# Kernel tuning notes

Hardware: AMD Instinct MI355X
Metric: run time of the kernel (lower is better)

The kernel has to match this reference:

```python
import jax, jax.numpy as jnp
import numpy as np

NUM_USR = 8192
H = 256  # NUM_SOURCE == H (feature dim of y_a); NUM_TARGET = 256


def setup_inputs() -> dict:
    key = jax.random.key(0)
    k1, k2, k3, k4 = jax.random.split(key, 4)
    return {
        "y_a": jax.random.normal(k1, (NUM_USR, H), dtype=jnp.float32),
        "y_b": jax.random.normal(k2, (NUM_USR, H), dtype=jnp.float32),
        "W": jax.random.normal(k3, (H, H), dtype=jnp.float32) * (1.0 / np.sqrt(H)),
        "b": jax.random.normal(k4, (H,), dtype=jnp.float32) * 0.01,
    }


def reference(y_a, y_b, W, b):
    # Linear: proj[j] = W @ y_b[j] + b   (torch nn.Linear convention)
    proj = jnp.einsum("jt,st->js", y_b, W) + b          # [num_usr, H]
    # torch loop computes score[i, j] = y_a[i] . proj[j], replicated H times
    # then averaged: out[i, k] = (1/H) * sum_j sigmoid(score[i, j])
    scores = jnp.einsum("ih,jh->ij", y_a, proj)          # [num_usr, num_usr]
    s = jnp.sum(jax.nn.sigmoid(scores), axis=1) / y_a.shape[1]  # [num_usr]
    return jnp.broadcast_to(s[:, None], y_a.shape)       # [num_usr, H]
```

## Files before the change

### kernel.cpp

```cpp
#include <hip/hip_runtime.h>

#define NUSR 8192
#define HDIM 256

typedef __attribute__((ext_vector_type(8))) __bf16 bf16x8;
typedef __attribute__((ext_vector_type(4))) float f32x4;

union frag_u { bf16x8 v; unsigned short u[8]; };

__device__ __forceinline__ unsigned short f2bf(float f) {
  unsigned u = __builtin_bit_cast(unsigned, f);
  u += 0x7FFFu + ((u >> 16) & 1u);
  return (unsigned short)(u >> 16);
}

__device__ __forceinline__ float sigmoidf_fast(float x) {
  float e = __builtin_amdgcn_exp2f(x * -1.44269504088896340736f);
  return __builtin_amdgcn_rcpf(1.0f + e);
}

__global__ __launch_bounds__(256) void k1_proj(
    const float* __restrict__ yb, const float* __restrict__ W,
    const float* __restrict__ bvec, unsigned short* __restrict__ Pbf)
{
  const int tid  = threadIdx.x;
  const int lane = tid & 63;
  const int w    = tid >> 6;
  const int quad = lane >> 4;
  const int l15  = lane & 15;
  const int rb   = blockIdx.x * 32;

  frag_u A[2][8];
#pragma unroll
  for (int h = 0; h < 2; ++h) {
    const float* src = yb + (size_t)(rb + h * 16 + l15) * HDIM;
#pragma unroll
    for (int kb = 0; kb < 8; ++kb) {
      float4 v0 = *(const float4*)&src[kb * 32 + quad * 8];
      float4 v1 = *(const float4*)&src[kb * 32 + quad * 8 + 4];
      A[h][kb].u[0] = f2bf(v0.x); A[h][kb].u[1] = f2bf(v0.y);
      A[h][kb].u[2] = f2bf(v0.z); A[h][kb].u[3] = f2bf(v0.w);
      A[h][kb].u[4] = f2bf(v1.x); A[h][kb].u[5] = f2bf(v1.y);
      A[h][kb].u[6] = f2bf(v1.z); A[h][kb].u[7] = f2bf(v1.w);
    }
  }

#pragma unroll
  for (int tt = 0; tt < 4; ++tt) {
    const int scol = w * 64 + tt * 16 + l15;
    const float* wrow = W + (size_t)scol * HDIM;
    f32x4 a0 = {0.f,0.f,0.f,0.f}, a1 = {0.f,0.f,0.f,0.f};
#pragma unroll
    for (int kb = 0; kb < 8; ++kb) {
      float4 v0 = *(const float4*)&wrow[kb * 32 + quad * 8];
      float4 v1 = *(const float4*)&wrow[kb * 32 + quad * 8 + 4];
      frag_u B;
      B.u[0] = f2bf(v0.x); B.u[1] = f2bf(v0.y);
      B.u[2] = f2bf(v0.z); B.u[3] = f2bf(v0.w);
      B.u[4] = f2bf(v1.x); B.u[5] = f2bf(v1.y);
      B.u[6] = f2bf(v1.z); B.u[7] = f2bf(v1.w);
      a0 = __builtin_amdgcn_mfma_f32_16x16x32_bf16(A[0][kb].v, B.v, a0, 0, 0, 0);
      a1 = __builtin_amdgcn_mfma_f32_16x16x32_bf16(A[1][kb].v, B.v, a1, 0, 0, 0);
    }
    const float bcol = bvec[scol];
#pragma unroll
    for (int r = 0; r < 4; ++r) {
      Pbf[(size_t)(rb + quad * 4 + r) * HDIM + scol]      = f2bf(a0[r] + bcol);
      Pbf[(size_t)(rb + 16 + quad * 4 + r) * HDIM + scol] = f2bf(a1[r] + bcol);
    }
  }
}

__global__ __launch_bounds__(256) void k2_score(
    const float* __restrict__ ya, const unsigned short* __restrict__ Pbf,
    float* __restrict__ svec)
{
  __shared__ __align__(16) unsigned short bs[64 * 264];
  const int tid  = threadIdx.x;
  const int lane = tid & 63;
  const int w    = tid >> 6;
  const int quad = lane >> 4;
  const int l15  = lane & 15;
  const int rbase = blockIdx.x * 128 + w * 32;
  const int cbase = blockIdx.y * 512;

  frag_u A[2][8];
#pragma unroll
  for (int h = 0; h < 2; ++h) {
    const float* src = ya + (size_t)(rbase + h * 16 + l15) * HDIM;
#pragma unroll
    for (int kb = 0; kb < 8; ++kb) {
      float4 v0 = *(const float4*)&src[kb * 32 + quad * 8];
      float4 v1 = *(const float4*)&src[kb * 32 + quad * 8 + 4];
      A[h][kb].u[0] = f2bf(v0.x); A[h][kb].u[1] = f2bf(v0.y);
      A[h][kb].u[2] = f2bf(v0.z); A[h][kb].u[3] = f2bf(v0.w);
      A[h][kb].u[4] = f2bf(v1.x); A[h][kb].u[5] = f2bf(v1.y);
      A[h][kb].u[6] = f2bf(v1.z); A[h][kb].u[7] = f2bf(v1.w);
    }
  }

  float rs[2][4] = {{0.f,0.f,0.f,0.f},{0.f,0.f,0.f,0.f}};

  for (int st = 0; st < 8; ++st) {
    __syncthreads();
    {
      const uint4* src = (const uint4*)(Pbf + (size_t)(cbase + st * 64) * HDIM);
#pragma unroll
      for (int p = 0; p < 8; ++p) {
        int lin = p * 256 + tid;
        int row = lin >> 5, ch = lin & 31;
        *(uint4*)&bs[row * 264 + ch * 8] = src[row * 32 + ch];
      }
    }
    __syncthreads();
#pragma unroll
    for (int tt = 0; tt < 4; ++tt) {
      f32x4 a0 = {0.f,0.f,0.f,0.f}, a1 = {0.f,0.f,0.f,0.f};
#pragma unroll
      for (int kb = 0; kb < 8; ++kb) {
        bf16x8 bfrag = *(const bf16x8*)&bs[(tt * 16 + l15) * 264 + kb * 32 + quad * 8];
        a0 = __builtin_amdgcn_mfma_f32_16x16x32_bf16(A[0][kb].v, bfrag, a0, 0, 0, 0);
        a1 = __builtin_amdgcn_mfma_f32_16x16x32_bf16(A[1][kb].v, bfrag, a1, 0, 0, 0);
      }
#pragma unroll
      for (int r = 0; r < 4; ++r) {
        rs[0][r] += sigmoidf_fast(a0[r]);
        rs[1][r] += sigmoidf_fast(a1[r]);
      }
    }
  }

#pragma unroll
  for (int off = 1; off < 16; off <<= 1) {
#pragma unroll
    for (int h = 0; h < 2; ++h)
#pragma unroll
      for (int r = 0; r < 4; ++r)
        rs[h][r] += __shfl_xor(rs[h][r], off, 64);
  }
  if (l15 == 0) {
#pragma unroll
    for (int h = 0; h < 2; ++h)
#pragma unroll
      for (int r = 0; r < 4; ++r)
        atomicAdd(&svec[rbase + h * 16 + quad * 4 + r], rs[h][r]);
  }
}

__global__ __launch_bounds__(256) void k3_bcast(
    const float* __restrict__ svec, float* __restrict__ out)
{
  int idx = blockIdx.x * 256 + threadIdx.x;
  int row = idx >> 6;
  float v = svec[row] * (1.0f / 256.0f);
  float4 o = {v, v, v, v};
  ((float4*)out)[idx] = o;
}

extern "C" void kernel_launch(void* const* d_in, const int* in_sizes, int n_in,
                              void* d_out, int out_size, void* d_ws, size_t ws_size,
                              hipStream_t stream) {
  (void)in_sizes; (void)n_in; (void)out_size;
  const float* ya = (const float*)d_in[0];
  const float* yb = (const float*)d_in[1];
  const float* W  = (const float*)d_in[2];
  const float* bv = (const float*)d_in[3];
  float* out = (float*)d_out;

  char* ws = (char*)d_ws;
  unsigned short* Pbf;
  float* svec;
  const size_t need = (4ull << 20) + (32ull << 10);
  if (ws_size >= need) {
    Pbf  = (unsigned short*)ws;
    svec = (float*)(ws + (4 << 20));
  } else {
    Pbf  = (unsigned short*)d_out;
    svec = (float*)ws;
  }

  hipMemsetAsync(svec, 0, NUSR * sizeof(float), stream);
  k1_proj<<<256, 256, 0, stream>>>(yb, W, bv, Pbf);
  k2_score<<<dim3(64, 16), 256, 0, stream>>>(ya, Pbf, svec);
  k3_bcast<<<2048, 256, 0, stream>>>(svec, out);
}
```

Before: 131.8 us.

## Enlarge score row tile, split projection grid, fold memset into projection kernel

The score kernel now has each wave cover 64 rows instead of 32, so every B fragment read from shared memory feeds four MFMAs instead of two. The grid is halved and each block stages the same number of columns, which cuts global and LDS traffic per useful FLOP. The projection kernel moves to a 2D grid with one output tile per wave, which raises parallelism. It also zeroes svec, removing the separate memset launch, and the bf16 packing now converts two values per 32-bit word. In exchange the score kernel uses more registers and launches only 512 blocks, so occupancy and load balance may drop.

```diff
diff --git a/kernel.cpp b/kernel.cpp
--- a/kernel.cpp
+++ b/kernel.cpp
@@ -6,12 +6,16 @@
 typedef __attribute__((ext_vector_type(8))) __bf16 bf16x8;
 typedef __attribute__((ext_vector_type(4))) float f32x4;
 
-union frag_u { bf16x8 v; unsigned short u[8]; };
+union frag_u { bf16x8 v; unsigned short u[8]; unsigned int d[4]; };
 
-__device__ __forceinline__ unsigned short f2bf(float f) {
+__device__ __forceinline__ unsigned int f2bf(float f) {
   unsigned u = __builtin_bit_cast(unsigned, f);
   u += 0x7FFFu + ((u >> 16) & 1u);
-  return (unsigned short)(u >> 16);
+  return u >> 16;
+}
+
+__device__ __forceinline__ unsigned int f2bf2(float lo, float hi) {
+  return f2bf(lo) | (f2bf(hi) << 16);
 }
 
 __device__ __forceinline__ float sigmoidf_fast(float x) {
@@ -21,7 +25,8 @@
 
 __global__ __launch_bounds__(256) void k1_proj(
     const float* __restrict__ yb, const float* __restrict__ W,
-    const float* __restrict__ bvec, unsigned short* __restrict__ Pbf)
+    const float* __restrict__ bvec, unsigned short* __restrict__ Pbf,
+    float* __restrict__ svec)
 {
   const int tid  = threadIdx.x;
   const int lane = tid & 63;
@@ -29,6 +34,9 @@
   const int quad = lane >> 4;
   const int l15  = lane & 15;
   const int rb   = blockIdx.x * 32;
+  const int sb   = blockIdx.y * 64 + w * 16;
+
+  if (blockIdx.y == 0 && tid < 32) svec[rb + tid] = 0.f;
 
   frag_u A[2][8];
 #pragma unroll
@@ -38,40 +46,36 @@
     for (int kb = 0; kb < 8; ++kb) {
       float4 v0 = *(const float4*)&src[kb * 32 + quad * 8];
       float4 v1 = *(const float4*)&src[kb * 32 + quad * 8 + 4];
-      A[h][kb].u[0] = f2bf(v0.x); A[h][kb].u[1] = f2bf(v0.y);
-      A[h][kb].u[2] = f2bf(v0.z); A[h][kb].u[3] = f2bf(v0.w);
-      A[h][kb].u[4] = f2bf(v1.x); A[h][kb].u[5] = f2bf(v1.y);
-      A[h][kb].u[6] = f2bf(v1.z); A[h][kb].u[7] = f2bf(v1.w);
+      A[h][kb].d[0] = f2bf2(v0.x, v0.y);
+      A[h][kb].d[1] = f2bf2(v0.z, v0.w);
+      A[h][kb].d[2] = f2bf2(v1.x, v1.y);
+      A[h][kb].d[3] = f2bf2(v1.z, v1.w);
     }
   }
 
+  const float* wrow = W + (size_t)(sb + l15) * HDIM;
+  f32x4 a0 = {0.f,0.f,0.f,0.f}, a1 = {0.f,0.f,0.f,0.f};
 #pragma unroll
-  for (int tt = 0; tt < 4; ++tt) {
-    const int scol = w * 64 + tt * 16 + l15;
-    const float* wrow = W + (size_t)scol * HDIM;
-    f32x4 a0 = {0.f,0.f,0.f,0.f}, a1 = {0.f,0.f,0.f,0.f};
+  for (int kb = 0; kb < 8; ++kb) {
+    float4 v0 = *(const float4*)&wrow[kb * 32 + quad * 8];
+    float4 v1 = *(const float4*)&wrow[kb * 32 + quad * 8 + 4];
+    frag_u B;
+    B.d[0] = f2bf2(v0.x, v0.y);
+    B.d[1] = f2bf2(v0.z, v0.w);
+    B.d[2] = f2bf2(v1.x, v1.y);
+    B.d[3] = f2bf2(v1.z, v1.w);
+    a0 = __builtin_amdgcn_mfma_f32_16x16x32_bf16(A[0][kb].v, B.v, a0, 0, 0, 0);
+    a1 = __builtin_amdgcn_mfma_f32_16x16x32_bf16(A[1][kb].v, B.v, a1, 0, 0, 0);
+  }
+  const float bias = bvec[sb + l15];
 #pragma unroll
-    for (int kb = 0; kb < 8; ++kb) {
-      float4 v0 = *(const float4*)&wrow[kb * 32 + quad * 8];
-      float4 v1 = *(const float4*)&wrow[kb * 32 + quad * 8 + 4];
-      frag_u B;
-      B.u[0] = f2bf(v0.x); B.u[1] = f2bf(v0.y);
-      B.u[2] = f2bf(v0.z); B.u[3] = f2bf(v0.w);
-      B.u[4] = f2bf(v1.x); B.u[5] = f2bf(v1.y);
-      B.u[6] = f2bf(v1.z); B.u[7] = f2bf(v1.w);
-      a0 = __builtin_amdgcn_mfma_f32_16x16x32_bf16(A[0][kb].v, B.v, a0, 0, 0, 0);
-      a1 = __builtin_amdgcn_mfma_f32_16x16x32_bf16(A[1][kb].v, B.v, a1, 0, 0, 0);
-    }
-    const float bcol = bvec[scol];
-#pragma unroll
-    for (int r = 0; r < 4; ++r) {
-      Pbf[(size_t)(rb + quad * 4 + r) * HDIM + scol]      = f2bf(a0[r] + bcol);
-      Pbf[(size_t)(rb + 16 + quad * 4 + r) * HDIM + scol] = f2bf(a1[r] + bcol);
-    }
+  for (int r = 0; r < 4; ++r) {
+    Pbf[(size_t)(rb + quad * 4 + r) * HDIM + sb + l15]      = (unsigned short)f2bf(a0[r] + bias);
+    Pbf[(size_t)(rb + 16 + quad * 4 + r) * HDIM + sb + l15] = (unsigned short)f2bf(a1[r] + bias);
   }
 }
 
-__global__ __launch_bounds__(256) void k2_score(
+__global__ __launch_bounds__(256, 2) void k2_score(
     const float* __restrict__ ya, const unsigned short* __restrict__ Pbf,
     float* __restrict__ svec)
 {
@@ -81,25 +85,26 @@
   const int w    = tid >> 6;
   const int quad = lane >> 4;
   const int l15  = lane & 15;
-  const int rbase = blockIdx.x * 128 + w * 32;
+  const int rbase = blockIdx.x * 256 + w * 64;
   const int cbase = blockIdx.y * 512;
 
-  frag_u A[2][8];
+  frag_u A[4][8];
 #pragma unroll
-  for (int h = 0; h < 2; ++h) {
-    const float* src = ya + (size_t)(rbase + h * 16 + l15) * HDIM;
+  for (int g = 0; g < 4; ++g) {
+    const float* src = ya + (size_t)(rbase + g * 16 + l15) * HDIM;
 #pragma unroll
     for (int kb = 0; kb < 8; ++kb) {
       float4 v0 = *(const float4*)&src[kb * 32 + quad * 8];
       float4 v1 = *(const float4*)&src[kb * 32 + quad * 8 + 4];
-      A[h][kb].u[0] = f2bf(v0.x); A[h][kb].u[1] = f2bf(v0.y);
-      A[h][kb].u[2] = f2bf(v0.z); A[h][kb].u[3] = f2bf(v0.w);
-      A[h][kb].u[4] = f2bf(v1.x); A[h][kb].u[5] = f2bf(v1.y);
-      A[h][kb].u[6] = f2bf(v1.z); A[h][kb].u[7] = f2bf(v1.w);
+      A[g][kb].d[0] = f2bf2(v0.x, v0.y);
+      A[g][kb].d[1] = f2bf2(v0.z, v0.w);
+      A[g][kb].d[2] = f2bf2(v1.x, v1.y);
+      A[g][kb].d[3] = f2bf2(v1.z, v1.w);
     }
   }
 
-  float rs[2][4] = {{0.f,0.f,0.f,0.f},{0.f,0.f,0.f,0.f}};
+  float rs[4][4] = {{0.f,0.f,0.f,0.f},{0.f,0.f,0.f,0.f},
+                    {0.f,0.f,0.f,0.f},{0.f,0.f,0.f,0.f}};
 
   for (int st = 0; st < 8; ++st) {
     __syncthreads();
@@ -115,35 +120,37 @@
     __syncthreads();
 #pragma unroll
     for (int tt = 0; tt < 4; ++tt) {
-      f32x4 a0 = {0.f,0.f,0.f,0.f}, a1 = {0.f,0.f,0.f,0.f};
+      f32x4 acc[4] = {{0.f,0.f,0.f,0.f},{0.f,0.f,0.f,0.f},
+                      {0.f,0.f,0.f,0.f},{0.f,0.f,0.f,0.f}};
 #pragma unroll
       for (int kb = 0; kb < 8; ++kb) {
         bf16x8 bfrag = *(const bf16x8*)&bs[(tt * 16 + l15) * 264 + kb * 32 + quad * 8];
-        a0 = __builtin_amdgcn_mfma_f32_16x16x32_bf16(A[0][kb].v, bfrag, a0, 0, 0, 0);
-        a1 = __builtin_amdgcn_mfma_f32_16x16x32_bf16(A[1][kb].v, bfrag, a1, 0, 0, 0);
+#pragma unroll
+        for (int g = 0; g < 4; ++g)
+          acc[g] = __builtin_amdgcn_mfma_f32_16x16x32_bf16(A[g][kb].v, bfrag, acc[g], 0, 0, 0);
       }
 #pragma unroll
-      for (int r = 0; r < 4; ++r) {
-        rs[0][r] += sigmoidf_fast(a0[r]);
-        rs[1][r] += sigmoidf_fast(a1[r]);
-      }
+      for (int g = 0; g < 4; ++g)
+#pragma unroll
+        for (int r = 0; r < 4; ++r)
+          rs[g][r] += sigmoidf_fast(acc[g][r]);
     }
   }
 
 #pragma unroll
-  for (int off = 1; off < 16; off <<= 1) {
+  for (int off = 1; off < 16; off <<= 1)
 #pragma unroll
-    for (int h = 0; h < 2; ++h)
+    for (int g = 0; g < 4; ++g)
 #pragma unroll
       for (int r = 0; r < 4; ++r)
-        rs[h][r] += __shfl_xor(rs[h][r], off, 64);
-  }
+        rs[g][r] += __shfl_xor(rs[g][r], off, 64);
+
   if (l15 == 0) {
 #pragma unroll
-    for (int h = 0; h < 2; ++h)
+    for (int g = 0; g < 4; ++g)
 #pragma unroll
       for (int r = 0; r < 4; ++r)
-        atomicAdd(&svec[rbase + h * 16 + quad * 4 + r], rs[h][r]);
+        atomicAdd(&svec[rbase + g * 16 + quad * 4 + r], rs[g][r]);
   }
 }
 
@@ -179,8 +186,7 @@
     svec = (float*)ws;
   }
 
-  hipMemsetAsync(svec, 0, NUSR * sizeof(float), stream);
-  k1_proj<<<256, 256, 0, stream>>>(yb, W, bv, Pbf);
-  k2_score<<<dim3(64, 16), 256, 0, stream>>>(ya, Pbf, svec);
+  k1_proj<<<dim3(256, 4), 256, 0, stream>>>(yb, W, bv, Pbf, svec);
+  k2_score<<<dim3(32, 16), 256, 0, stream>>>(ya, Pbf, svec);
   k3_bcast<<<2048, 256, 0, stream>>>(svec, out);
 }
```

Result: slower. 144.9 us (+9.9%).

## Pre-swizzle projection into MFMA fragment layout, pre-convert y_a, async LDS loads

Applied to the files above, without the earlier changes.

The projection kernel now writes P in a fragment-ordered layout so the score kernel can copy tiles into LDS with global_load_lds and read B fragments contiguously per lane. The same kernel converts y_a to bf16 once and zeroes svec, which removes the separate memset and the repeated f32-to-bf16 conversion across the 16 column blocks of the score kernel. The projection kernel is restructured into 512 single-wave blocks that compute W·y_b with y_b as the resident operand. The costs are an extra 4 MB workspace buffer and a dependence on the exact fragment layout matching between the two kernels.

```diff
diff --git a/kernel.cpp b/kernel.cpp
--- a/kernel.cpp
+++ b/kernel.cpp
@@ -6,111 +6,115 @@
 typedef __attribute__((ext_vector_type(8))) __bf16 bf16x8;
 typedef __attribute__((ext_vector_type(4))) float f32x4;
 
-union frag_u { bf16x8 v; unsigned short u[8]; };
+union frag_u { bf16x8 v; unsigned short u[8]; unsigned int d[4]; };
 
-__device__ __forceinline__ unsigned short f2bf(float f) {
+__device__ __forceinline__ unsigned int f2bf(float f) {
   unsigned u = __builtin_bit_cast(unsigned, f);
   u += 0x7FFFu + ((u >> 16) & 1u);
-  return (unsigned short)(u >> 16);
+  return u >> 16;
 }
-
+__device__ __forceinline__ unsigned int f2bf2(float lo, float hi) {
+  return f2bf(lo) | (f2bf(hi) << 16);
+}
 __device__ __forceinline__ float sigmoidf_fast(float x) {
   float e = __builtin_amdgcn_exp2f(x * -1.44269504088896340736f);
   return __builtin_amdgcn_rcpf(1.0f + e);
 }
 
-__global__ __launch_bounds__(256) void k1_proj(
-    const float* __restrict__ yb, const float* __restrict__ W,
-    const float* __restrict__ bvec, unsigned short* __restrict__ Pbf)
+
+__global__ __launch_bounds__(64) void k1_proj(
+    const float* __restrict__ ya, const float* __restrict__ yb,
+    const float* __restrict__ W, const float* __restrict__ bvec,
+    unsigned short* __restrict__ PX, unsigned short* __restrict__ yabf,
+    float* __restrict__ svec)
 {
-  const int tid  = threadIdx.x;
-  const int lane = tid & 63;
-  const int w    = tid >> 6;
-  const int quad = lane >> 4;
-  const int l15  = lane & 15;
-  const int rb   = blockIdx.x * 32;
+  const int lane = threadIdx.x;
+  const int q = lane >> 4, i = lane & 15;
+  const int jg = blockIdx.x;
 
-  frag_u A[2][8];
+  {
+    const float4* src = (const float4*)ya;
+    uint4* dst = (uint4*)yabf;
 #pragma unroll
-  for (int h = 0; h < 2; ++h) {
-    const float* src = yb + (size_t)(rb + h * 16 + l15) * HDIM;
+    for (int u = 0; u < 8; ++u) {
+      int d = u * 32768 + jg * 64 + lane;
+      float4 a = src[d * 2];
+      float4 b = src[d * 2 + 1];
+      uint4 o = { f2bf2(a.x, a.y), f2bf2(a.z, a.w),
+                  f2bf2(b.x, b.y), f2bf2(b.z, b.w) };
+      dst[d] = o;
+    }
+  }
+  if (jg < 128) svec[jg * 64 + lane] = 0.f;
+
+  frag_u B[8];
+  {
+    const float* ybrow = yb + (size_t)(jg * 16 + i) * HDIM;
 #pragma unroll
     for (int kb = 0; kb < 8; ++kb) {
-      float4 v0 = *(const float4*)&src[kb * 32 + quad * 8];
-      float4 v1 = *(const float4*)&src[kb * 32 + quad * 8 + 4];
-      A[h][kb].u[0] = f2bf(v0.x); A[h][kb].u[1] = f2bf(v0.y);
-      A[h][kb].u[2] = f2bf(v0.z); A[h][kb].u[3] = f2bf(v0.w);
-      A[h][kb].u[4] = f2bf(v1.x); A[h][kb].u[5] = f2bf(v1.y);
-      A[h][kb].u[6] = f2bf(v1.z); A[h][kb].u[7] = f2bf(v1.w);
+      float4 v0 = *(const float4*)&ybrow[kb * 32 + q * 8];
+      float4 v1 = *(const float4*)&ybrow[kb * 32 + q * 8 + 4];
+      B[kb].d[0] = f2bf2(v0.x, v0.y); B[kb].d[1] = f2bf2(v0.z, v0.w);
+      B[kb].d[2] = f2bf2(v1.x, v1.y); B[kb].d[3] = f2bf2(v1.z, v1.w);
     }
   }
 
-#pragma unroll
-  for (int tt = 0; tt < 4; ++tt) {
-    const int scol = w * 64 + tt * 16 + l15;
-    const float* wrow = W + (size_t)scol * HDIM;
-    f32x4 a0 = {0.f,0.f,0.f,0.f}, a1 = {0.f,0.f,0.f,0.f};
+#pragma unroll 2
+  for (int st = 0; st < 16; ++st) {
+    f32x4 acc = {0.f, 0.f, 0.f, 0.f};
 #pragma unroll
     for (int kb = 0; kb < 8; ++kb) {
-      float4 v0 = *(const float4*)&wrow[kb * 32 + quad * 8];
-      float4 v1 = *(const float4*)&wrow[kb * 32 + quad * 8 + 4];
-      frag_u B;
-      B.u[0] = f2bf(v0.x); B.u[1] = f2bf(v0.y);
-      B.u[2] = f2bf(v0.z); B.u[3] = f2bf(v0.w);
-      B.u[4] = f2bf(v1.x); B.u[5] = f2bf(v1.y);
-      B.u[6] = f2bf(v1.z); B.u[7] = f2bf(v1.w);
-      a0 = __builtin_amdgcn_mfma_f32_16x16x32_bf16(A[0][kb].v, B.v, a0, 0, 0, 0);
-      a1 = __builtin_amdgcn_mfma_f32_16x16x32_bf16(A[1][kb].v, B.v, a1, 0, 0, 0);
+      const float* wrow = W + (size_t)(st * 16 + i) * HDIM + kb * 32 + q * 8;
+      float4 w0 = *(const float4*)wrow;
+      float4 w1 = *(const float4*)(wrow + 4);
+      frag_u Af;
+      Af.d[0] = f2bf2(w0.x, w0.y); Af.d[1] = f2bf2(w0.z, w0.w);
+      Af.d[2] = f2bf2(w1.x, w1.y); Af.d[3] = f2bf2(w1.z, w1.w);
+      acc = __builtin_amdgcn_mfma_f32_16x16x32_bf16(Af.v, B[kb].v, acc, 0, 0, 0);
     }
-    const float bcol = bvec[scol];
-#pragma unroll
-    for (int r = 0; r < 4; ++r) {
-      Pbf[(size_t)(rb + quad * 4 + r) * HDIM + scol]      = f2bf(a0[r] + bcol);
-      Pbf[(size_t)(rb + 16 + quad * 4 + r) * HDIM + scol] = f2bf(a1[r] + bcol);
-    }
+    float4 bias = *(const float4*)&bvec[st * 16 + q * 4];
+    unsigned v0 = f2bf2(acc[0] + bias.x, acc[1] + bias.y);
+    unsigned v1 = f2bf2(acc[2] + bias.z, acc[3] + bias.w);
+    size_t off = (size_t)jg * 4096 + (size_t)(st >> 1) * 512
+               + (size_t)(((st & 1) << 1) | (q >> 1)) * 128 + i * 8 + ((q & 1) * 4);
+    *(uint2*)(PX + off) = make_uint2(v0, v1);
   }
 }
 
 __global__ __launch_bounds__(256) void k2_score(
-    const float* __restrict__ ya, const unsigned short* __restrict__ Pbf,
+    const unsigned short* __restrict__ yabf, const unsigned short* __restrict__ PX,
     float* __restrict__ svec)
 {
-  __shared__ __align__(16) unsigned short bs[64 * 264];
+  __shared__ __align__(16) unsigned short bs[16384];
   const int tid  = threadIdx.x;
   const int lane = tid & 63;
   const int w    = tid >> 6;
   const int quad = lane >> 4;
   const int l15  = lane & 15;
   const int rbase = blockIdx.x * 128 + w * 32;
-  const int cbase = blockIdx.y * 512;
+  const int cg16  = blockIdx.y * 32;
 
   frag_u A[2][8];
 #pragma unroll
   for (int h = 0; h < 2; ++h) {
-    const float* src = ya + (size_t)(rbase + h * 16 + l15) * HDIM;
+    const unsigned short* src = yabf + (size_t)(rbase + h * 16 + l15) * HDIM;
 #pragma unroll
-    for (int kb = 0; kb < 8; ++kb) {
-      float4 v0 = *(const float4*)&src[kb * 32 + quad * 8];
-      float4 v1 = *(const float4*)&src[kb * 32 + quad * 8 + 4];
-      A[h][kb].u[0] = f2bf(v0.x); A[h][kb].u[1] = f2bf(v0.y);
-      A[h][kb].u[2] = f2bf(v0.z); A[h][kb].u[3] = f2bf(v0.w);
-      A[h][kb].u[4] = f2bf(v1.x); A[h][kb].u[5] = f2bf(v1.y);
-      A[h][kb].u[6] = f2bf(v1.z); A[h][kb].u[7] = f2bf(v1.w);
-    }
+    for (int kb = 0; kb < 8; ++kb)
+      A[h][kb].v = *(const bf16x8*)&src[kb * 32 + quad * 8];
   }
 
   float rs[2][4] = {{0.f,0.f,0.f,0.f},{0.f,0.f,0.f,0.f}};
 
   for (int st = 0; st < 8; ++st) {
+    const unsigned short* src = PX + (size_t)(cg16 + st * 4) * 4096;
     __syncthreads();
-    {
-      const uint4* src = (const uint4*)(Pbf + (size_t)(cbase + st * 64) * HDIM);
 #pragma unroll
-      for (int p = 0; p < 8; ++p) {
-        int lin = p * 256 + tid;
-        int row = lin >> 5, ch = lin & 31;
-        *(uint4*)&bs[row * 264 + ch * 8] = src[row * 32 + ch];
-      }
+    for (int p = 0; p < 8; ++p) {
+      int c = p * 256 + tid;
+      __builtin_amdgcn_global_load_lds(
+          (const __attribute__((address_space(1))) unsigned int*)(const void*)(src + c * 8),
+          (__attribute__((address_space(3))) unsigned int*)(void*)(bs + c * 8),
+          16, 0, 0);
     }
     __syncthreads();
 #pragma unroll
@@ -118,7 +122,7 @@
       f32x4 a0 = {0.f,0.f,0.f,0.f}, a1 = {0.f,0.f,0.f,0.f};
 #pragma unroll
       for (int kb = 0; kb < 8; ++kb) {
-        bf16x8 bfrag = *(const bf16x8*)&bs[(tt * 16 + l15) * 264 + kb * 32 + quad * 8];
+        bf16x8 bfrag = *(const bf16x8*)&bs[(tt * 512 + kb * 64 + lane) * 8];
         a0 = __builtin_amdgcn_mfma_f32_16x16x32_bf16(A[0][kb].v, bfrag, a0, 0, 0, 0);
         a1 = __builtin_amdgcn_mfma_f32_16x16x32_bf16(A[1][kb].v, bfrag, a1, 0, 0, 0);
       }
@@ -131,13 +135,13 @@
   }
 
 #pragma unroll
-  for (int off = 1; off < 16; off <<= 1) {
+  for (int off = 1; off < 16; off <<= 1)
 #pragma unroll
     for (int h = 0; h < 2; ++h)
 #pragma unroll
       for (int r = 0; r < 4; ++r)
         rs[h][r] += __shfl_xor(rs[h][r], off, 64);
-  }
+
   if (l15 == 0) {
 #pragma unroll
     for (int h = 0; h < 2; ++h)
@@ -168,19 +172,20 @@
   float* out = (float*)d_out;
 
   char* ws = (char*)d_ws;
-  unsigned short* Pbf;
+  unsigned short *PX, *yabf;
   float* svec;
-  const size_t need = (4ull << 20) + (32ull << 10);
+  const size_t need = (8ull << 20) + (32ull << 10);
   if (ws_size >= need) {
-    Pbf  = (unsigned short*)ws;
-    svec = (float*)(ws + (4 << 20));
+    PX   = (unsigned short*)ws;
+    yabf = (unsigned short*)(ws + (4 << 20));
+    svec = (float*)(ws + (8 << 20));
   } else {
-    Pbf  = (unsigned short*)d_out;
+    PX   = (unsigned short*)d_out;
+    yabf = (unsigned short*)((char*)d_out + (4 << 20));
     svec = (float*)ws;
   }
 
-  hipMemsetAsync(svec, 0, NUSR * sizeof(float), stream);
-  k1_proj<<<256, 256, 0, stream>>>(yb, W, bv, Pbf);
-  k2_score<<<dim3(64, 16), 256, 0, stream>>>(ya, Pbf, svec);
+  k1_proj<<<512, 64, 0, stream>>>(ya, yb, W, bv, PX, yabf, svec);
+  k2_score<<<dim3(64, 16), 256, 0, stream>>>(yabf, PX, svec);
   k3_bcast<<<2048, 256, 0, stream>>>(svec, out);
 }
```

Measured after the change: 165.3 us. +25.4%, slower.
